# Performance work log

Hardware: AMD Instinct MI355X
Metric: run time of the kernel (lower is better)

Reference implementation:

```python
import jax, jax.numpy as jnp
import numpy as np
from jax import lax

B, T, V, E, H, O = 32, 64, 30000, 64, 64, 7


def setup_inputs() -> dict:
    key = jax.random.key(0)
    ks = jax.random.split(key, 17)
    s_in = 1.0 / np.sqrt(E)
    s_h = 1.0 / np.sqrt(H)
    inp = {
        "x": jax.random.uniform(ks[0], (B, T, V), dtype=jnp.float32),
        "vocab_embed": 0.02 * jax.random.normal(ks[1], (V, E), dtype=jnp.float32),
        "W_ir": s_in * jax.random.normal(ks[2], (H, E), dtype=jnp.float32),
        "W_iz": s_in * jax.random.normal(ks[3], (H, E), dtype=jnp.float32),
        "W_in": s_in * jax.random.normal(ks[4], (H, E), dtype=jnp.float32),
        "W_hr": s_h * jax.random.normal(ks[5], (H, H), dtype=jnp.float32),
        "W_hz": s_h * jax.random.normal(ks[6], (H, H), dtype=jnp.float32),
        "W_hn": s_h * jax.random.normal(ks[7], (H, H), dtype=jnp.float32),
        "b_ir": s_h * jax.random.normal(ks[8], (H,), dtype=jnp.float32),
        "b_iz": s_h * jax.random.normal(ks[9], (H,), dtype=jnp.float32),
        "b_in": s_h * jax.random.normal(ks[10], (H,), dtype=jnp.float32),
        "b_hr": s_h * jax.random.normal(ks[11], (H,), dtype=jnp.float32),
        "b_hz": s_h * jax.random.normal(ks[12], (H,), dtype=jnp.float32),
        "b_hn": s_h * jax.random.normal(ks[13], (H,), dtype=jnp.float32),
        "W_out": s_h * jax.random.normal(ks[14], (O, H), dtype=jnp.float32),
        "b_out": s_h * jax.random.normal(ks[15], (O,), dtype=jnp.float32),
        "prediction_point": T,
    }
    return inp


def reference(x, vocab_embed, W_ir, W_iz, W_in, W_hr, W_hz, W_hn,
              b_ir, b_iz, b_in, b_hr, b_hz, b_hn, W_out, b_out,
              prediction_point):
    # embed_x = relu((x @ vocab_embed) / x.sum(-1, keepdims))  -> [B, T, E]
    embed_x = jax.nn.relu(jnp.einsum("btv,ve->bte", x, vocab_embed)
                          / jnp.sum(x, axis=2, keepdims=True))

    # t = 0: no hidden contribution at all (faithful to original)
    e0 = embed_x[:, 0, :]
    z1 = jax.nn.sigmoid(e0 @ W_iz.T + b_iz)
    n1 = jnp.tanh(e0 @ W_in.T + b_in)
    h0 = (1.0 - z1) * n1  # [B, H]

    def step(h, e_t):
        hr = h @ W_hr.T + b_hr
        r = jax.nn.sigmoid(e_t @ W_ir.T + b_ir + hr)
        z = jax.nn.sigmoid(e_t @ W_iz.T + b_iz + h @ W_hz.T + b_hz)
        # NOTE: original code uses hidden_reset (W_hr) here, not hidden_new
        n = jnp.tanh(e_t @ W_in.T + b_in + r * hr)
        h_new = (1.0 - z) * n + z * h
        return h_new, None

    # scan over t = 1 .. prediction_point-1
    es = jnp.swapaxes(embed_x[:, 1:prediction_point, :], 0, 1)  # [T-1, B, E]
    h_final, _ = lax.scan(step, h0, es)

    return h_final @ W_out.T + b_out  # [B, O] logits (prob=False)
```

## Files before the change

### kernel.cpp

```cpp
#include <hip/hip_runtime.h>
#include <hip/hip_bf16.h>

typedef unsigned short u16;
typedef short short8 __attribute__((ext_vector_type(8)));
typedef float floatx4 __attribute__((ext_vector_type(4)));

#define BB 32
#define TT 64
#define VV 30000
#define EE 64
#define HH 64
#define OO 7
#define KSPLIT 32
#define NU32 937

__device__ __forceinline__ u16 f2b(float f) {
    unsigned u = __float_as_uint(f);
    u += 0x7FFFu + ((u >> 16) & 1u);
    return (u16)(u >> 16);
}

__device__ __forceinline__ unsigned pk2(float fo, float fe) {
    return __builtin_amdgcn_perm(__float_as_uint(fo), __float_as_uint(fe), 0x07060302u);
}

__device__ __forceinline__ float sigmoid_f(float x) {
    return 1.f / (1.f + __expf(-x));
}

__device__ __forceinline__ float tanh_f(float x) {
    float a = fabsf(x);
    float e = __expf(-2.f * a);
    float t = (1.f - e) / (1.f + e);
    return x < 0.f ? -t : t;
}

__global__ __launch_bounds__(256) void kT(const float* __restrict__ VE, u16* __restrict__ VTf) {
    __shared__ u16 tile[64][72];
    int v0 = blockIdx.x * 64;
    int t = threadIdx.x;
    #pragma unroll
    for (int it = 0; it < 4; ++it) {
        int c = it * 256 + t;
        int row = c >> 4, col4 = (c & 15) * 4;
        ushort4 s; s.x = 0; s.y = 0; s.z = 0; s.w = 0;
        if (v0 + row < VV) {
            float4 d = *(const float4*)(VE + (size_t)(v0 + row) * EE + col4);
            s.x = f2b(d.x); s.y = f2b(d.y); s.z = f2b(d.z); s.w = f2b(d.w);
        }
        *(ushort4*)&tile[row][col4] = s;
    }
    __syncthreads();
    int e = t & 63;
    int nb = e >> 4, r = e & 15;
    #pragma unroll
    for (int half = 0; half < 2; ++half) {
        int q8 = (t >> 6) + half * 4;
        int u = (v0 >> 5) + (q8 >> 2);
        int kin = (q8 & 3) * 8;
        u16 tmp[8];
        #pragma unroll
        for (int jj = 0; jj < 8; ++jj) tmp[jj] = tile[q8 * 8 + jj][e];
        *(uint4*)&VTf[(size_t)u * 2048 + nb * 512 + r * 32 + kin] = *(uint4*)tmp;
    }
}

__global__ __launch_bounds__(256) void kE(const float* __restrict__ x, const u16* __restrict__ vtf,
                                          float* __restrict__ Cpart, float* __restrict__ Rpart) {
    int tid = threadIdx.x;
    int w = tid >> 6, l = tid & 63;
    int r15 = l & 15, q = l >> 4;
    int mb = blockIdx.x, kb = blockIdx.y;
    int m0 = mb * 64;
    int wr = m0 + w * 16;
    int u0 = (kb * NU32) / KSPLIT, u1 = ((kb + 1) * NU32) / KSPLIT;

    const float* aP = x + (size_t)(wr + r15) * VV + u0 * 32 + q * 8;
    const u16*   bP = vtf + (size_t)u0 * 2048 + r15 * 32 + q * 8;

    floatx4 acc[4] = {};
    floatx4 accS = {};
    short8 ones;
    #pragma unroll
    for (int i = 0; i < 8; ++i) ones[i] = (short)0x3F80;

    #pragma unroll 2
    for (int u = u0; u < u1; ++u) {
        float4 a0 = *(const float4*)(aP);
        float4 a1 = *(const float4*)(aP + 4);
        short8 bf0 = *(const short8*)(bP);
        short8 bf1 = *(const short8*)(bP + 512);
        short8 bf2 = *(const short8*)(bP + 1024);
        short8 bf3 = *(const short8*)(bP + 1536);
        short8 af;
        unsigned* afu = (unsigned*)&af;
        afu[0] = pk2(a0.y, a0.x);
        afu[1] = pk2(a0.w, a0.z);
        afu[2] = pk2(a1.y, a1.x);
        afu[3] = pk2(a1.w, a1.z);
        acc[0] = __builtin_amdgcn_mfma_f32_16x16x32_bf16(af, bf0, acc[0], 0, 0, 0);
        acc[1] = __builtin_amdgcn_mfma_f32_16x16x32_bf16(af, bf1, acc[1], 0, 0, 0);
        acc[2] = __builtin_amdgcn_mfma_f32_16x16x32_bf16(af, bf2, acc[2], 0, 0, 0);
        acc[3] = __builtin_amdgcn_mfma_f32_16x16x32_bf16(af, bf3, acc[3], 0, 0, 0);
        accS   = __builtin_amdgcn_mfma_f32_16x16x32_bf16(af, ones, accS, 0, 0, 0);
        aP += 32;
        bP += 2048;
    }

    if (kb == KSPLIT - 1) {
        short8 af;
        #pragma unroll
        for (int i = 0; i < 8; ++i) af[i] = 0;
        if (q < 2) {
            float4 a0 = *(const float4*)(aP);
            float4 a1 = *(const float4*)(aP + 4);
            unsigned* afu = (unsigned*)&af;
            afu[0] = pk2(a0.y, a0.x);
            afu[1] = pk2(a0.w, a0.z);
            afu[2] = pk2(a1.y, a1.x);
            afu[3] = pk2(a1.w, a1.z);
        }
        short8 bf0 = *(const short8*)(bP);
        short8 bf1 = *(const short8*)(bP + 512);
        short8 bf2 = *(const short8*)(bP + 1024);
        short8 bf3 = *(const short8*)(bP + 1536);
        acc[0] = __builtin_amdgcn_mfma_f32_16x16x32_bf16(af, bf0, acc[0], 0, 0, 0);
        acc[1] = __builtin_amdgcn_mfma_f32_16x16x32_bf16(af, bf1, acc[1], 0, 0, 0);
        acc[2] = __builtin_amdgcn_mfma_f32_16x16x32_bf16(af, bf2, acc[2], 0, 0, 0);
        acc[3] = __builtin_amdgcn_mfma_f32_16x16x32_bf16(af, bf3, acc[3], 0, 0, 0);
        accS   = __builtin_amdgcn_mfma_f32_16x16x32_bf16(af, ones, accS, 0, 0, 0);
    }

    float* Cp = Cpart + (size_t)kb * (2048 * 64);
    #pragma unroll
    for (int r = 0; r < 4; ++r) {
        int row = wr + q * 4 + r;
        #pragma unroll
        for (int n = 0; n < 4; ++n)
            Cp[(size_t)row * 64 + n * 16 + r15] = acc[n][r];
        if (r15 == 0) Rpart[kb * 2048 + row] = accS[r];
    }
}

__global__ __launch_bounds__(256) void kG2(const float* __restrict__ Cpart, const float* __restrict__ Rpart,
                                           const float* __restrict__ Wir, const float* __restrict__ Wiz,
                                           const float* __restrict__ Win,
                                           const float* __restrict__ bir, const float* __restrict__ biz,
                                           const float* __restrict__ bin,
                                           float* __restrict__ Xr, float* __restrict__ Xz,
                                           float* __restrict__ Xn, float* __restrict__ H0) {
    __shared__ __align__(16) u16 eL[64 * 72];
    __shared__ float rsinv[64];
    int tid = threadIdx.x;
    int m0 = blockIdx.x * 64;

    if (tid < 64) {
        float rs = 0.f;
        #pragma unroll
        for (int kb = 0; kb < KSPLIT; ++kb)
            rs += Rpart[kb * 2048 + m0 + tid];
        rsinv[tid] = 1.f / rs;
    }
    float4 a4[4];
    #pragma unroll
    for (int r = 0; r < 4; ++r) { a4[r].x = 0.f; a4[r].y = 0.f; a4[r].z = 0.f; a4[r].w = 0.f; }
    const float* cp = Cpart + (size_t)m0 * 64 + tid * 4;
    #pragma unroll 4
    for (int kb = 0; kb < KSPLIT; ++kb) {
        #pragma unroll
        for (int r = 0; r < 4; ++r) {
            float4 v = *(const float4*)(cp + (size_t)kb * (2048 * 64) + r * 1024);
            a4[r].x += v.x; a4[r].y += v.y; a4[r].z += v.z; a4[r].w += v.w;
        }
    }
    __syncthreads();
    #pragma unroll
    for (int r = 0; r < 4; ++r) {
        int m = r * 16 + (tid >> 4);
        float ri = rsinv[m];
        float e0 = a4[r].x * ri, e1 = a4[r].y * ri, e2 = a4[r].z * ri, e3 = a4[r].w * ri;
        e0 = e0 > 0.f ? e0 : 0.f;  e1 = e1 > 0.f ? e1 : 0.f;
        e2 = e2 > 0.f ? e2 : 0.f;  e3 = e3 > 0.f ? e3 : 0.f;
        ushort4 s;
        s.x = f2b(e0); s.y = f2b(e1); s.z = f2b(e2); s.w = f2b(e3);
        *(ushort4*)&eL[m * 72 + (tid & 15) * 4] = s;
    }
    __syncthreads();

    int w = tid >> 6, l = tid & 63;
    int r15 = l & 15, q = l >> 4;
    short8 a0 = *(const short8*)&eL[(w * 16 + r15) * 72 + q * 8];
    short8 a1 = *(const short8*)&eL[(w * 16 + r15) * 72 + 32 + q * 8];

    floatx4 acc[3][4] = {};
    #pragma unroll
    for (int g = 0; g < 3; ++g) {
        const float* W = (g == 0) ? Wir : (g == 1) ? Wiz : Win;
        #pragma unroll
        for (int nb = 0; nb < 4; ++nb) {
            const float* wrow = W + (nb * 16 + r15) * 64 + q * 8;
            float4 w0 = *(const float4*)(wrow);
            float4 w1 = *(const float4*)(wrow + 4);
            float4 w2 = *(const float4*)(wrow + 32);
            float4 w3 = *(const float4*)(wrow + 36);
            short8 b0, b1;
            unsigned* b0u = (unsigned*)&b0; unsigned* b1u = (unsigned*)&b1;
            b0u[0] = pk2(w0.y, w0.x); b0u[1] = pk2(w0.w, w0.z);
            b0u[2] = pk2(w1.y, w1.x); b0u[3] = pk2(w1.w, w1.z);
            b1u[0] = pk2(w2.y, w2.x); b1u[1] = pk2(w2.w, w2.z);
            b1u[2] = pk2(w3.y, w3.x); b1u[3] = pk2(w3.w, w3.z);
            acc[g][nb] = __builtin_amdgcn_mfma_f32_16x16x32_bf16(a0, b0, acc[g][nb], 0, 0, 0);
            acc[g][nb] = __builtin_amdgcn_mfma_f32_16x16x32_bf16(a1, b1, acc[g][nb], 0, 0, 0);
        }
    }

    #pragma unroll
    for (int g = 0; g < 3; ++g) {
        float* Xo = (g == 0) ? Xr : (g == 1) ? Xz : Xn;
        const float* bo = (g == 0) ? bir : (g == 1) ? biz : bin;
        #pragma unroll
        for (int nb = 0; nb < 4; ++nb) {
            int j = nb * 16 + r15;
            float bias = bo[j];
            #pragma unroll
            for (int r = 0; r < 4; ++r) {
                int m = m0 + w * 16 + q * 4 + r;
                Xo[(size_t)m * 64 + j] = acc[g][nb][r] + bias;
            }
        }
    }
    if (w == 0 && q == 0) {
        #pragma unroll
        for (int nb = 0; nb < 4; ++nb) {
            int j = nb * 16 + r15;
            float z1 = sigmoid_f(acc[1][nb][0] + biz[j]);
            float n1 = tanh_f(acc[2][nb][0] + bin[j]);
            H0[blockIdx.x * 64 + j] = (1.f - z1) * n1;
        }
    }
}

__global__ __launch_bounds__(64) void kS2(const float* __restrict__ Xr, const float* __restrict__ Xz,
                                          const float* __restrict__ Xn, const float* __restrict__ H0,
                                          const float* __restrict__ Whr, const float* __restrict__ Whz,
                                          const float* __restrict__ bhr, const float* __restrict__ bhz,
                                          const float* __restrict__ Wout, const float* __restrict__ bout,
                                          float* __restrict__ out) {
    int b = blockIdx.x;
    int i = threadIdx.x;
    __shared__ float Xs[3][64][64];
    __shared__ float hsh[64];

    const float* s0 = Xr + (size_t)b * 4096;
    const float* s1 = Xz + (size_t)b * 4096;
    const float* s2 = Xn + (size_t)b * 4096;
    #pragma unroll
    for (int c = 0; c < 16; ++c) {
        int off = (c * 64 + i) * 4;
        *(float4*)&Xs[0][0][off] = *(const float4*)(s0 + off);
        *(float4*)&Xs[1][0][off] = *(const float4*)(s1 + off);
        *(float4*)&Xs[2][0][off] = *(const float4*)(s2 + off);
    }
    float wrg[64], wzg[64];
    #pragma unroll
    for (int c = 0; c < 16; ++c) {
        float4 v1 = *(const float4*)(Whr + i * 64 + c * 4);
        float4 v2 = *(const float4*)(Whz + i * 64 + c * 4);
        wrg[c * 4 + 0] = v1.x; wrg[c * 4 + 1] = v1.y; wrg[c * 4 + 2] = v1.z; wrg[c * 4 + 3] = v1.w;
        wzg[c * 4 + 0] = v2.x; wzg[c * 4 + 1] = v2.y; wzg[c * 4 + 2] = v2.z; wzg[c * 4 + 3] = v2.w;
    }
    float h = H0[b * 64 + i];
    float bri = bhr[i], bzi = bhz[i];

    for (int t = 1; t < 64; ++t) {
        float xr = Xs[0][t][i], xz = Xs[1][t][i], xn = Xs[2][t][i];
        float p0 = 0.f, p1 = 0.f, p2 = 0.f, p3 = 0.f;
        float z0 = 0.f, z1 = 0.f, z2 = 0.f, z3 = 0.f;
        unsigned hu = __float_as_uint(h);
        #pragma unroll
        for (int j = 0; j < 64; j += 4) {
            float h0 = __uint_as_float(__builtin_amdgcn_readlane(hu, j + 0));
            float h1 = __uint_as_float(__builtin_amdgcn_readlane(hu, j + 1));
            float h2 = __uint_as_float(__builtin_amdgcn_readlane(hu, j + 2));
            float h3 = __uint_as_float(__builtin_amdgcn_readlane(hu, j + 3));
            p0 += h0 * wrg[j + 0]; p1 += h1 * wrg[j + 1];
            p2 += h2 * wrg[j + 2]; p3 += h3 * wrg[j + 3];
            z0 += h0 * wzg[j + 0]; z1 += h1 * wzg[j + 1];
            z2 += h2 * wzg[j + 2]; z3 += h3 * wzg[j + 3];
        }
        float hr = bri + ((p0 + p1) + (p2 + p3));
        float hz = bzi + ((z0 + z1) + (z2 + z3));
        float r = sigmoid_f(xr + hr);
        float z = sigmoid_f(xz + hz);
        float n = tanh_f(xn + r * hr);
        h = (1.f - z) * n + z * h;
    }

    hsh[i] = h;
    __syncthreads();
    if (i < OO) {
        float a = bout[i];
        #pragma unroll 8
        for (int j = 0; j < 64; ++j)
            a += hsh[j] * Wout[i * 64 + j];
        out[b * OO + i] = a;
    }
}

extern "C" void kernel_launch(void* const* d_in, const int* in_sizes, int n_in,
                              void* d_out, int out_size, void* d_ws, size_t ws_size,
                              hipStream_t stream) {
    const float* x    = (const float*)d_in[0];
    const float* VE   = (const float*)d_in[1];
    const float* Wir  = (const float*)d_in[2];
    const float* Wiz  = (const float*)d_in[3];
    const float* Win  = (const float*)d_in[4];
    const float* Whr  = (const float*)d_in[5];
    const float* Whz  = (const float*)d_in[6];
    const float* bir  = (const float*)d_in[8];
    const float* biz  = (const float*)d_in[9];
    const float* bin  = (const float*)d_in[10];
    const float* bhr  = (const float*)d_in[11];
    const float* bhz  = (const float*)d_in[12];
    const float* Wout = (const float*)d_in[14];
    const float* bout = (const float*)d_in[15];

    char* ws = (char*)d_ws;
    u16*   VTf   = (u16*)(ws);
    float* Cpart = (float*)(ws + 4000000);
    float* Rpart = (float*)(ws + 20777216);
    float* Xr    = (float*)(ws + 21039360);
    float* Xz    = (float*)(ws + 21563648);
    float* Xn    = (float*)(ws + 22087936);
    float* H0    = (float*)(ws + 22612224);

    kT<<<469, 256, 0, stream>>>(VE, VTf);
    kE<<<dim3(2048 / 64, KSPLIT), 256, 0, stream>>>(x, VTf, Cpart, Rpart);
    kG2<<<32, 256, 0, stream>>>(Cpart, Rpart, Wir, Wiz, Win, bir, biz, bin, Xr, Xz, Xn, H0);
    kS2<<<BB, 64, 0, stream>>>(Xr, Xz, Xn, H0, Whr, Whz, bhr, bhz, Wout, bout, (float*)d_out);
}
```

Before: 435.3 us.

## Fuse input-gate projection and GRU recurrence into one kernel via shared memory

Merges the gate-projection kernel and the sequential GRU scan kernel so the projected gate inputs and initial hidden state stay in shared memory instead of round-tripping through global memory, and drops one launch. The recurrence then runs on the first wavefront of the 256-thread block while the other waves exit. It also raises the unroll factor of the main embedding GEMM loop from 2 to 4. The larger shared memory footprint per block and the higher register pressure from unrolling are the tradeoffs.

```diff
diff --git a/kernel.cpp b/kernel.cpp
--- a/kernel.cpp
+++ b/kernel.cpp
@@ -84,7 +84,7 @@
     #pragma unroll
     for (int i = 0; i < 8; ++i) ones[i] = (short)0x3F80;
 
-    #pragma unroll 2
+    #pragma unroll 4
     for (int u = u0; u < u1; ++u) {
         float4 a0 = *(const float4*)(aP);
         float4 a1 = *(const float4*)(aP + 4);
@@ -142,17 +142,22 @@
     }
 }
 
-__global__ __launch_bounds__(256) void kG2(const float* __restrict__ Cpart, const float* __restrict__ Rpart,
+__global__ __launch_bounds__(256) void kGS(const float* __restrict__ Cpart, const float* __restrict__ Rpart,
                                            const float* __restrict__ Wir, const float* __restrict__ Wiz,
                                            const float* __restrict__ Win,
                                            const float* __restrict__ bir, const float* __restrict__ biz,
                                            const float* __restrict__ bin,
-                                           float* __restrict__ Xr, float* __restrict__ Xz,
-                                           float* __restrict__ Xn, float* __restrict__ H0) {
+                                           const float* __restrict__ Whr, const float* __restrict__ Whz,
+                                           const float* __restrict__ bhr, const float* __restrict__ bhz,
+                                           const float* __restrict__ Wout, const float* __restrict__ bout,
+                                           float* __restrict__ out) {
     __shared__ __align__(16) u16 eL[64 * 72];
     __shared__ float rsinv[64];
+    __shared__ float Xs[3][64][64];
+    __shared__ float hsh[64];
     int tid = threadIdx.x;
-    int m0 = blockIdx.x * 64;
+    int b = blockIdx.x;
+    int m0 = b * 64;
 
     if (tid < 64) {
         float rs = 0.f;
@@ -189,8 +194,8 @@
 
     int w = tid >> 6, l = tid & 63;
     int r15 = l & 15, q = l >> 4;
-    short8 a0 = *(const short8*)&eL[(w * 16 + r15) * 72 + q * 8];
-    short8 a1 = *(const short8*)&eL[(w * 16 + r15) * 72 + 32 + q * 8];
+    short8 fa0 = *(const short8*)&eL[(w * 16 + r15) * 72 + q * 8];
+    short8 fa1 = *(const short8*)&eL[(w * 16 + r15) * 72 + 32 + q * 8];
 
     floatx4 acc[3][4] = {};
     #pragma unroll
@@ -209,14 +214,13 @@
             b0u[2] = pk2(w1.y, w1.x); b0u[3] = pk2(w1.w, w1.z);
             b1u[0] = pk2(w2.y, w2.x); b1u[1] = pk2(w2.w, w2.z);
             b1u[2] = pk2(w3.y, w3.x); b1u[3] = pk2(w3.w, w3.z);
-            acc[g][nb] = __builtin_amdgcn_mfma_f32_16x16x32_bf16(a0, b0, acc[g][nb], 0, 0, 0);
-            acc[g][nb] = __builtin_amdgcn_mfma_f32_16x16x32_bf16(a1, b1, acc[g][nb], 0, 0, 0);
+            acc[g][nb] = __builtin_amdgcn_mfma_f32_16x16x32_bf16(fa0, b0, acc[g][nb], 0, 0, 0);
+            acc[g][nb] = __builtin_amdgcn_mfma_f32_16x16x32_bf16(fa1, b1, acc[g][nb], 0, 0, 0);
         }
     }
 
     #pragma unroll
     for (int g = 0; g < 3; ++g) {
-        float* Xo = (g == 0) ? Xr : (g == 1) ? Xz : Xn;
         const float* bo = (g == 0) ? bir : (g == 1) ? biz : bin;
         #pragma unroll
         for (int nb = 0; nb < 4; ++nb) {
@@ -224,8 +228,8 @@
             float bias = bo[j];
             #pragma unroll
             for (int r = 0; r < 4; ++r) {
-                int m = m0 + w * 16 + q * 4 + r;
-                Xo[(size_t)m * 64 + j] = acc[g][nb][r] + bias;
+                int t = w * 16 + q * 4 + r;
+                Xs[g][t][j] = acc[g][nb][r] + bias;
             }
         }
     }
@@ -235,32 +239,13 @@
             int j = nb * 16 + r15;
             float z1 = sigmoid_f(acc[1][nb][0] + biz[j]);
             float n1 = tanh_f(acc[2][nb][0] + bin[j]);
-            H0[blockIdx.x * 64 + j] = (1.f - z1) * n1;
-        }
-    }
-}
-
-__global__ __launch_bounds__(64) void kS2(const float* __restrict__ Xr, const float* __restrict__ Xz,
-                                          const float* __restrict__ Xn, const float* __restrict__ H0,
-                                          const float* __restrict__ Whr, const float* __restrict__ Whz,
-                                          const float* __restrict__ bhr, const float* __restrict__ bhz,
-                                          const float* __restrict__ Wout, const float* __restrict__ bout,
-                                          float* __restrict__ out) {
-    int b = blockIdx.x;
-    int i = threadIdx.x;
-    __shared__ float Xs[3][64][64];
-    __shared__ float hsh[64];
-
-    const float* s0 = Xr + (size_t)b * 4096;
-    const float* s1 = Xz + (size_t)b * 4096;
-    const float* s2 = Xn + (size_t)b * 4096;
-    #pragma unroll
-    for (int c = 0; c < 16; ++c) {
-        int off = (c * 64 + i) * 4;
-        *(float4*)&Xs[0][0][off] = *(const float4*)(s0 + off);
-        *(float4*)&Xs[1][0][off] = *(const float4*)(s1 + off);
-        *(float4*)&Xs[2][0][off] = *(const float4*)(s2 + off);
-    }
+            hsh[j] = (1.f - z1) * n1;
+        }
+    }
+    __syncthreads();
+
+    if (tid >= 64) return;
+    int i = tid;
     float wrg[64], wzg[64];
     #pragma unroll
     for (int c = 0; c < 16; ++c) {
@@ -269,7 +254,7 @@
         wrg[c * 4 + 0] = v1.x; wrg[c * 4 + 1] = v1.y; wrg[c * 4 + 2] = v1.z; wrg[c * 4 + 3] = v1.w;
         wzg[c * 4 + 0] = v2.x; wzg[c * 4 + 1] = v2.y; wzg[c * 4 + 2] = v2.z; wzg[c * 4 + 3] = v2.w;
     }
-    float h = H0[b * 64 + i];
+    float h = hsh[i];
     float bri = bhr[i], bzi = bhz[i];
 
     for (int t = 1; t < 64; ++t) {
@@ -297,7 +282,6 @@
     }
 
     hsh[i] = h;
-    __syncthreads();
     if (i < OO) {
         float a = bout[i];
         #pragma unroll 8
@@ -329,13 +313,9 @@
     u16*   VTf   = (u16*)(ws);
     float* Cpart = (float*)(ws + 4000000);
     float* Rpart = (float*)(ws + 20777216);
-    float* Xr    = (float*)(ws + 21039360);
-    float* Xz    = (float*)(ws + 21563648);
-    float* Xn    = (float*)(ws + 22087936);
-    float* H0    = (float*)(ws + 22612224);
 
     kT<<<469, 256, 0, stream>>>(VE, VTf);
     kE<<<dim3(2048 / 64, KSPLIT), 256, 0, stream>>>(x, VTf, Cpart, Rpart);
-    kG2<<<32, 256, 0, stream>>>(Cpart, Rpart, Wir, Wiz, Win, bir, biz, bin, Xr, Xz, Xn, H0);
-    kS2<<<BB, 64, 0, stream>>>(Xr, Xz, Xn, H0, Whr, Whz, bhr, bhz, Wout, bout, (float*)d_out);
-}
+    kGS<<<BB, 256, 0, stream>>>(Cpart, Rpart, Wir, Wiz, Win, bir, biz, bin,
+                                Whr, Whz, bhr, bhz, Wout, bout, (float*)d_out);
+}
```

After: 423.3 us. 2.7% less time.
